# Performance work log

Measured on AMD Instinct MI355X. Metric: run time of the kernel, lower is better.

The kernel has to match this reference:

```python
import jax, jax.numpy as jnp
import numpy as np

B, C, H, W, HEADS = 8, 256, 64, 64, 4
EPS = 1e-5  # torch InstanceNorm2d default eps


def conv1x1(x, w):
    # w: [out_c, in_c]; x: [b, in_c, h, w]
    return jnp.einsum('oc,bchw->bohw', w, x)


def maxpool2(x):
    b, c, h, w = x.shape
    return x.reshape(b, c, h // 2, 2, w // 2, 2).max(axis=(3, 5))


def inorm_affine(x, g, b):
    # InstanceNorm2d(affine=True): normalize per (batch, channel) over H,W
    m = jnp.mean(x, axis=(2, 3), keepdims=True)
    v = jnp.mean((x - m) ** 2, axis=(2, 3), keepdims=True)
    return (x - m) * jax.lax.rsqrt(v + EPS) * g[None, :, None, None] + b[None, :, None, None]


def setup_inputs() -> dict:
    key = jax.random.key(0)
    ks = jax.random.split(key, 12)
    s = 1.0 / np.sqrt(C)  # fan-in style scaling for 1x1 conv weights
    return {
        'x': jax.random.normal(ks[0], (B, C, H, W), jnp.float32),
        'theta_w': jax.random.normal(ks[1], (C, C), jnp.float32) * s,
        'phi_w': jax.random.normal(ks[2], (C, C), jnp.float32) * s,
        'g_w': jax.random.normal(ks[3], (C // 2, C), jnp.float32) * s,
        'o_w': jax.random.normal(ks[4], (C, C // 2), jnp.float32) * np.sqrt(2.0 / C),
        'nt_w': 1.0 + 0.1 * jax.random.normal(ks[5], (C,), jnp.float32),
        'nt_b': 0.1 * jax.random.normal(ks[6], (C,), jnp.float32),
        'np_w': 1.0 + 0.1 * jax.random.normal(ks[7], (C,), jnp.float32),
        'np_b': 0.1 * jax.random.normal(ks[8], (C,), jnp.float32),
        'ng_w': 1.0 + 0.1 * jax.random.normal(ks[9], (C // 2,), jnp.float32),
        'ng_b': 0.1 * jax.random.normal(ks[10], (C // 2,), jnp.float32),
        'gamma': jnp.float32(0.5),
    }


def reference(x, theta_w, phi_w, g_w, o_w, nt_w, nt_b, np_w, np_b, ng_w, ng_b, gamma):
    b, c, h, w = x.shape
    n = h * w            # query length
    m = n // 4           # key/value length after 2x2 maxpool
    theta = inorm_affine(conv1x1(x, theta_w), nt_w, nt_b)
    phi = inorm_affine(maxpool2(conv1x1(x, phi_w)), np_w, np_b)
    g = inorm_affine(maxpool2(conv1x1(x, g_w)), ng_w, ng_b)
    # custom head layout: channel dim split as (C//heads, heads), head dim INNER
    theta_ = theta.reshape(b, c // HEADS, HEADS, n)
    phi_ = phi.reshape(b, c // HEADS, HEADS, m)
    g_ = g.reshape(b, (c // 2) // HEADS, HEADS, m)
    beta = jax.nn.softmax(jnp.einsum('bchi,bchj->bhij', theta_, phi_), axis=-1)
    o = jnp.einsum('bchj,bhij->bchi', g_, beta).reshape(b, c // 2, h, w)
    o = conv1x1(o, o_w)
    return gamma * o + x
```

## Files before the change

### kernel.cpp

```cpp
#include <hip/hip_runtime.h>
#include <hip/hip_bf16.h>
#include <math.h>

typedef float f32x4 __attribute__((ext_vector_type(4)));
typedef float f32x16 __attribute__((ext_vector_type(16)));
typedef __bf16 b16x8 __attribute__((ext_vector_type(8)));
typedef __bf16 b16x4 __attribute__((ext_vector_type(4)));
typedef unsigned int u32x2 __attribute__((ext_vector_type(2)));
typedef unsigned int u32x4 __attribute__((ext_vector_type(4)));

#define L2E 1.44269504088896340736f

__global__ void prep_weights(const float* tw, const float* pw, const float* gw,
                             const float* ow, __bf16* Wp, __bf16* OWp) {
    int idx = blockIdx.x * 256 + threadIdx.x;
    if (idx < 640 * 256) {
        int m = idx >> 8, k = idx & 255;
        float v;
        if (m < 256)      { int o = ((m & 63) << 2) + (m >> 6);            v = tw[o * 256 + k]; }
        else if (m < 512) { int mm = m - 256; int o = ((mm & 63) << 2) + (mm >> 6); v = pw[o * 256 + k]; }
        else              { int mm = m - 512; int o = ((mm & 31) << 2) + (mm >> 5); v = gw[o * 256 + k]; }
        Wp[idx] = (__bf16)v;
    } else {
        int j = idx - 640 * 256;
        if (j < 256 * 128) {
            int m = j >> 7, c = j & 127;
            int o = ((c & 31) << 2) + (c >> 5);
            OWp[j] = (__bf16)ow[m * 128 + o];
        }
    }
}

__global__ __launch_bounds__(256) void conv_gemm(const __bf16* __restrict__ Wp,
                                                 const float* __restrict__ x,
                                                 __bf16* theta_t, __bf16* phk, __bf16* gT,
                                                 float* tp1, float* tp2,
                                                 float* pp1, float* pp2,
                                                 float* gp1, float* gp2) {
    __shared__ __align__(16) char smem[38912];
    __bf16* Al = (__bf16*)smem;
    __bf16* Bl = (__bf16*)(smem + 10240);
    __bf16* Pl = (__bf16*)smem;
    float* S1w = (float*)(smem + 34816);
    float* S2w = (float*)(smem + 36864);
    int b = blockIdx.z, mt = blockIdx.y, nt = blockIdx.x;
    int tid = threadIdx.x, l = tid & 63, w = tid >> 6;
    int wm = w >> 1, wn = w & 1, lr = l & 15, lg = l >> 4;
    f32x4 acc[4][4];
#pragma unroll
    for (int i = 0; i < 4; i++)
#pragma unroll
        for (int j = 0; j < 4; j++)
#pragma unroll
            for (int r = 0; r < 4; r++) acc[i][j][r] = 0.f;
    const __bf16* Ag = Wp + (size_t)mt * 128 * 256;
    const float* Bx = x + (size_t)b * 1048576 + nt * 128;
    int srow = tid >> 2, scol = (tid & 3) * 8;
    int bn = tid & 127, bk0 = (tid >> 7) * 8;
    b16x8 aR[2];
    float xr[2][8];
#pragma unroll
    for (int hh = 0; hh < 2; hh++)
        aR[hh] = *(const b16x8*)&Ag[(size_t)(srow + hh * 64) * 256 + scol];
#pragma unroll
    for (int u = 0; u < 2; u++)
#pragma unroll
        for (int e = 0; e < 8; e++)
            xr[u][e] = Bx[(size_t)(bk0 + u * 16 + e) * 4096 + bn];
    for (int k0 = 0; k0 < 256; k0 += 32) {
        if (k0) __syncthreads();
#pragma unroll
        for (int hh = 0; hh < 2; hh++)
            *(b16x8*)&Al[(srow + hh * 64) * 40 + scol] = aR[hh];
#pragma unroll
        for (int u = 0; u < 2; u++) {
            b16x8 v;
#pragma unroll
            for (int e = 0; e < 8; e++) v[e] = (__bf16)xr[u][e];
            *(b16x8*)&Bl[bn * 40 + bk0 + u * 16] = v;
        }
        __syncthreads();
        if (k0 < 224) {
#pragma unroll
            for (int hh = 0; hh < 2; hh++)
                aR[hh] = *(const b16x8*)&Ag[(size_t)(srow + hh * 64) * 256 + k0 + 32 + scol];
#pragma unroll
            for (int u = 0; u < 2; u++)
#pragma unroll
                for (int e = 0; e < 8; e++)
                    xr[u][e] = Bx[(size_t)(k0 + 32 + bk0 + u * 16 + e) * 4096 + bn];
        }
        int ko = lg * 8;
        b16x8 af[4], bfr[4];
#pragma unroll
        for (int i = 0; i < 4; i++) af[i]  = *(b16x8*)&Al[(wm * 64 + i * 16 + lr) * 40 + ko];
#pragma unroll
        for (int i = 0; i < 4; i++) bfr[i] = *(b16x8*)&Bl[(wn * 64 + i * 16 + lr) * 40 + ko];
#pragma unroll
        for (int i = 0; i < 4; i++)
#pragma unroll
            for (int j = 0; j < 4; j++)
                acc[i][j] = __builtin_amdgcn_mfma_f32_16x16x32_bf16(af[i], bfr[j], acc[i][j], 0, 0, 0);
    }
    if (mt < 2) {
#pragma unroll
        for (int i = 0; i < 4; i++) {
            float s1v[4], s2v[4];
#pragma unroll
            for (int r = 0; r < 4; r++) {
                float a0 = acc[i][0][r], a1 = acc[i][1][r], a2 = acc[i][2][r], a3 = acc[i][3][r];
                s1v[r] = (a0 + a1) + (a2 + a3);
                s2v[r] = (a0 * a0 + a1 * a1) + (a2 * a2 + a3 * a3);
            }
#pragma unroll
            for (int msk = 1; msk < 16; msk <<= 1)
#pragma unroll
                for (int r = 0; r < 4; r++) {
                    s1v[r] += __shfl_xor(s1v[r], msk, 64);
                    s2v[r] += __shfl_xor(s2v[r], msk, 64);
                }
            if (lr == 0) {
                int row = (b * 32 + nt) * 2 + wn;
#pragma unroll
                for (int r = 0; r < 4; r++) {
                    int ch = mt * 128 + wm * 64 + i * 16 + lg * 4 + r;
                    tp1[row * 256 + ch] = s1v[r];
                    tp2[row * 256 + ch] = s2v[r];
                }
            }
        }
        int rbase = lg * 4;
#pragma unroll
        for (int i = 0; i < 4; i++) {
            int m = mt * 128 + wm * 64 + i * 16 + rbase;
#pragma unroll
            for (int j = 0; j < 4; j++) {
                int p = nt * 128 + wn * 64 + j * 16 + lr;
                b16x4 v;
#pragma unroll
                for (int r = 0; r < 4; r++) v[r] = (__bf16)acc[i][j][r];
                *(b16x4*)&theta_t[((size_t)b * 4096 + p) * 256 + m] = v;
            }
        }
    } else {
        __syncthreads();
        int rbase = lg * 4;
#pragma unroll
        for (int i = 0; i < 4; i++) {
            int ch = wm * 64 + i * 16 + rbase;
#pragma unroll
            for (int j = 0; j < 4; j++) {
                int p = wn * 64 + j * 16 + lr;
                b16x4 v;
#pragma unroll
                for (int r = 0; r < 4; r++) v[r] = (__bf16)acc[i][j][r];
                *(b16x4*)&Pl[p * 136 + ch] = v;
            }
        }
        __syncthreads();
        int o = tid & 15, tq = tid >> 4;
        float a1[8], a2[8];
#pragma unroll
        for (int e = 0; e < 8; e++) { a1[e] = 0.f; a2[e] = 0.f; }
        b16x8 pooled[2];
#pragma unroll
        for (int ss = 0; ss < 2; ss++) {
            int xq = tq * 2 + ss;
            b16x8 v0 = *(b16x8*)&Pl[(2 * xq) * 136 + o * 8];
            b16x8 v1 = *(b16x8*)&Pl[(2 * xq + 1) * 136 + o * 8];
            b16x8 v2 = *(b16x8*)&Pl[(64 + 2 * xq) * 136 + o * 8];
            b16x8 v3 = *(b16x8*)&Pl[(65 + 2 * xq) * 136 + o * 8];
            b16x8 mv;
#pragma unroll
            for (int e = 0; e < 8; e++) {
                float m = fmaxf(fmaxf((float)v0[e], (float)v1[e]), fmaxf((float)v2[e], (float)v3[e]));
                mv[e] = (__bf16)m; a1[e] += m; a2[e] += m * m;
            }
            pooled[ss] = mv;
        }
#pragma unroll
        for (int e = 0; e < 8; e++) {
            a1[e] += __shfl_xor(a1[e], 16, 64); a1[e] += __shfl_xor(a1[e], 32, 64);
            a2[e] += __shfl_xor(a2[e], 16, 64); a2[e] += __shfl_xor(a2[e], 32, 64);
        }
        if ((tid & 63) < 16) {
#pragma unroll
            for (int e = 0; e < 8; e++) {
                S1w[w * 128 + o * 8 + e] = a1[e];
                S2w[w * 128 + o * 8 + e] = a2[e];
            }
        }
        __syncthreads();
        int cc = nt >> 1;
        if (mt < 4) {
            if (tid < 128) {
                float s1 = S1w[tid] + S1w[128 + tid] + S1w[256 + tid] + S1w[384 + tid];
                float s2 = S2w[tid] + S2w[128 + tid] + S2w[256 + tid] + S2w[384 + tid];
                pp1[(size_t)(b * 32 + nt) * 256 + (mt - 2) * 128 + tid] = s1;
                pp2[(size_t)(b * 32 + nt) * 256 + (mt - 2) * 128 + tid] = s2;
            }
            int hh = (mt - 2) * 2 + (o >> 3), slot = o & 7, bh = b * 4 + hh;
#pragma unroll
            for (int ss = 0; ss < 2; ss++) {
                int key = (nt & 1) * 32 + tq * 2 + ss;
                *(b16x8*)&phk[((((size_t)bh * 16 + cc) * 8 + slot) * 64 + key) * 8] = pooled[ss];
            }
        } else {
            if (tid < 128) {
                float s1 = S1w[tid] + S1w[128 + tid] + S1w[256 + tid] + S1w[384 + tid];
                float s2 = S2w[tid] + S2w[128 + tid] + S2w[256 + tid] + S2w[384 + tid];
                gp1[(size_t)(b * 32 + nt) * 128 + tid] = s1;
                gp2[(size_t)(b * 32 + nt) * 128 + tid] = s2;
            }
            __bf16* Pg = Pl;
#pragma unroll
            for (int ss = 0; ss < 2; ss++)
                *(b16x8*)&Pg[(tq * 2 + ss) * 136 + o * 8] = pooled[ss];
            __syncthreads();
            int ch = tid & 127, kg = tid >> 7;
            int hh = ch >> 5, c32 = ch & 31, bh = b * 4 + hh;
#pragma unroll
            for (int gi = 0; gi < 2; gi++) {
                int g2 = kg * 2 + gi;
                b16x8 v;
#pragma unroll
                for (int e = 0; e < 8; e++) v[e] = Pg[(g2 * 8 + e) * 136 + ch];
                int seg = (nt & 1) * 4 + g2;
                *(b16x8*)&gT[((((size_t)bh * 16 + cc) * 8 + seg) * 32 + c32) * 8] = v;
            }
        }
    }
}

__global__ void finalize_stats(const float* tp1, const float* tp2, const float* pp1,
                               const float* pp2, const float* gp1, const float* gp2,
                               const float* ntw, const float* ntb, const float* npw,
                               const float* npb, const float* ngw, const float* ngb,
                               float* sct, float* bit, float* scp, float* bip,
                               float* scg, float* big) {
    int idx = blockIdx.x * 256 + threadIdx.x;
    if (idx >= 8 * 640) return;
    int b = idx / 640, c = idx % 640;
    if (c < 256) {
        float s1 = 0.f, s2 = 0.f;
        for (int i = 0; i < 64; i++) { s1 += tp1[(b * 64 + i) * 256 + c]; s2 += tp2[(b * 64 + i) * 256 + c]; }
        float n = 4096.f;
        float m = s1 / n, v = s2 / n - m * m;
        float r = rsqrtf(v + 1e-5f);
        int o = ((c & 63) << 2) + (c >> 6);
        float wv = ntw[o], bv = ntb[o];
        sct[b * 256 + c] = r * wv * L2E;
        bit[b * 256 + c] = (bv - m * r * wv) * L2E;
    } else if (c < 512) {
        int cc = c - 256;
        float s1 = 0.f, s2 = 0.f;
        for (int i = 0; i < 32; i++) { s1 += pp1[(b * 32 + i) * 256 + cc]; s2 += pp2[(b * 32 + i) * 256 + cc]; }
        float n = 1024.f;
        float m = s1 / n, v = s2 / n - m * m;
        float r = rsqrtf(v + 1e-5f);
        int o = ((cc & 63) << 2) + (cc >> 6);
        float wv = npw[o], bv = npb[o];
        scp[b * 256 + cc] = r * wv; bip[b * 256 + cc] = bv - m * r * wv;
    } else {
        int cc = c - 512;
        float s1 = 0.f, s2 = 0.f;
        for (int i = 0; i < 32; i++) { s1 += gp1[(b * 32 + i) * 128 + cc]; s2 += gp2[(b * 32 + i) * 128 + cc]; }
        float n = 1024.f;
        float m = s1 / n, v = s2 / n - m * m;
        float r = rsqrtf(v + 1e-5f);
        int o = ((cc & 31) << 2) + (cc >> 5);
        float wv = ngw[o], bv = ngb[o];
        scg[b * 128 + cc] = r * wv; big[b * 128 + cc] = bv - m * r * wv;
    }
}

__global__ void normalize_phk(__bf16* __restrict__ phk,
                              const float* __restrict__ scp,
                              const float* __restrict__ bip) {
    int u = blockIdx.x * 256 + threadIdx.x;
    int bh = u >> 13, slot = (u >> 6) & 7;
    int b = bh >> 2, h = bh & 3;
    int cf = b * 256 + h * 64 + (slot >> 1) * 16 + (slot & 1) * 8;
    size_t off = (size_t)u * 8;
    b16x8 v = *(b16x8*)&phk[off];
    b16x8 nv;
#pragma unroll
    for (int e = 0; e < 8; e++)
        nv[e] = (__bf16)((float)v[e] * scp[cf + e] + bip[cf + e]);
    *(b16x8*)&phk[off] = nv;
}

__global__ __launch_bounds__(256, 2) void attn(const __bf16* __restrict__ theta_t,
                                               const __bf16* __restrict__ phk,
                                               const __bf16* __restrict__ gTz,
                                               const float* __restrict__ sct,
                                               const float* __restrict__ bit,
                                               const float* __restrict__ scg,
                                               const float* __restrict__ big,
                                               __bf16* __restrict__ o_mid) {
    int bid = blockIdx.x;
    int idx = bid >> 3;
    int bh = (bid & 7) * 4 + (idx >> 4), qt = idx & 15;
    int b = bh >> 2, h = bh & 3;
    int tid = threadIdx.x, w = tid >> 6, lane = tid & 63;
    int l31 = lane & 31, hi = lane >> 5;
    int qb = qt * 256 + w * 64;

    b16x8 qf[2][4];
#pragma unroll
    for (int m = 0; m < 2; m++) {
        int q = qb + m * 32 + l31;
        const __bf16* qp = theta_t + ((size_t)b * 4096 + q) * 256 + h * 64;
#pragma unroll
        for (int st = 0; st < 4; st++) {
            int cb = st * 16 + hi * 8;
            b16x8 raw = *(const b16x8*)&qp[cb];
            b16x8 nv;
#pragma unroll
            for (int e = 0; e < 8; e++) {
                int cix = b * 256 + h * 64 + cb + e;
                nv[e] = (__bf16)((float)raw[e] * sct[cix] + bit[cix]);
            }
            qf[m][st] = nv;
        }
    }

    const __bf16* Kg = phk + (size_t)bh * 65536 + (size_t)hi * 512 + (size_t)l31 * 8;
    const __bf16* Vg = gTz + (size_t)bh * 32768 + (size_t)hi * 256 + (size_t)l31 * 8;

    f32x16 oacc[2];
    float l_run[2] = {0.f, 0.f};
#pragma unroll
    for (int m = 0; m < 2; m++)
#pragma unroll
        for (int r = 0; r < 16; r++) oacc[m][r] = 0.f;
    f32x16 zc;
#pragma unroll
    for (int r = 0; r < 16; r++) zc[r] = 0.f;

    b16x8 akA[2][4], avA[4], akB[2][4], avB[4];

#define LOADK(dst, c) { _Pragma("unroll") for (int kf = 0; kf < 2; kf++) \
    _Pragma("unroll") for (int st = 0; st < 4; st++) \
        dst[kf][st] = *(const b16x8*)&Kg[(size_t)(c) * 4096 + st * 1024 + kf * 256]; }
#define LOADV(dst, c) { _Pragma("unroll") for (int js = 0; js < 4; js++) \
    dst[js] = *(const b16x8*)&Vg[(size_t)(c) * 2048 + js * 512]; }
#define COMPUTE(ak, av) { \
    _Pragma("unroll") for (int m = 0; m < 2; m++) { \
        _Pragma("unroll") for (int kf = 0; kf < 2; kf++) { \
            f32x16 s = __builtin_amdgcn_mfma_f32_32x32x16_bf16(ak[kf][0], qf[m][0], zc, 0, 0, 0); \
            _Pragma("unroll") for (int st = 1; st < 4; st++) \
                s = __builtin_amdgcn_mfma_f32_32x32x16_bf16(ak[kf][st], qf[m][st], s, 0, 0, 0); \
            float sum = 0.f; \
            _Pragma("unroll") for (int r = 0; r < 16; r++) { \
                float p = __builtin_amdgcn_exp2f(s[r]); s[r] = p; sum += p; } \
            l_run[m] += sum; \
            _Pragma("unroll") for (int hh2 = 0; hh2 < 2; hh2++) { \
                b16x4 A4, B4; \
                _Pragma("unroll") for (int e = 0; e < 4; e++) { \
                    A4[e] = (__bf16)s[hh2 * 8 + e]; B4[e] = (__bf16)s[hh2 * 8 + 4 + e]; } \
                u32x2 a2 = __builtin_bit_cast(u32x2, A4); \
                u32x2 b2 = __builtin_bit_cast(u32x2, B4); \
                u32x2 q0 = __builtin_amdgcn_permlane32_swap(a2[0], b2[0], false, false); \
                u32x2 q1 = __builtin_amdgcn_permlane32_swap(a2[1], b2[1], false, false); \
                u32x4 pd = {q0[0], q1[0], q0[1], q1[1]}; \
                b16x8 pf = __builtin_bit_cast(b16x8, pd); \
                oacc[m] = __builtin_amdgcn_mfma_f32_32x32x16_bf16(av[kf * 2 + hh2], pf, oacc[m], 0, 0, 0); \
            } \
        } \
    } }

    LOADK(akA, 0) LOADV(avA, 0)
#pragma unroll 1
    for (int c = 0; c < 16; c += 2) {
        LOADK(akB, c + 1) LOADV(avB, c + 1)
        COMPUTE(akA, avA)
        if (c + 2 < 16) { LOADK(akA, c + 2) LOADV(avA, c + 2) }
        COMPUTE(akB, avB)
    }
#undef LOADK
#undef LOADV
#undef COMPUTE

#pragma unroll
    for (int m = 0; m < 2; m++) {
        float lr = l_run[m] + __shfl_xor(l_run[m], 32, 64);
        float rl = 1.0f / lr;
        int q = qb + m * 32 + l31;
#pragma unroll
        for (int rr = 0; rr < 4; rr++) {
            b16x4 v;
#pragma unroll
            for (int e = 0; e < 4; e++) {
                int ci = b * 128 + h * 32 + rr * 8 + hi * 4 + e;
                v[e] = (__bf16)(oacc[m][rr * 4 + e] * rl * scg[ci] + big[ci]);
            }
            *(b16x4*)&o_mid[((size_t)b * 4096 + q) * 128 + h * 32 + rr * 8 + hi * 4] = v;
        }
    }
}

__global__ __launch_bounds__(256) void out_gemm(const __bf16* __restrict__ OWp,
                                                const __bf16* __restrict__ o_mid,
                                                const float* __restrict__ x,
                                                const float* gamma, float* out) {
    int b = blockIdx.z, mt = blockIdx.y, nt = blockIdx.x;
    __shared__ __bf16 Al[128 * 40];
    __shared__ __bf16 Bl[128 * 40];
    int tid = threadIdx.x, l = tid & 63, w = tid >> 6;
    int wm = w >> 1, wn = w & 1, lr = l & 15, lg = l >> 4;
    f32x4 acc[4][4];
#pragma unroll
    for (int i = 0; i < 4; i++)
#pragma unroll
        for (int j = 0; j < 4; j++)
#pragma unroll
            for (int r = 0; r < 4; r++) acc[i][j][r] = 0.f;
    const __bf16* Ag = OWp + (size_t)mt * 128 * 128;
    const __bf16* Bg = o_mid + ((size_t)b * 4096 + nt * 128) * 128;
    int srow = tid >> 2, scol = (tid & 3) * 8;
    b16x8 aR[2], bR[2];
#pragma unroll
    for (int hh = 0; hh < 2; hh++) {
        int r = srow + hh * 64;
        aR[hh] = *(const b16x8*)&Ag[(size_t)r * 128 + scol];
        bR[hh] = *(const b16x8*)&Bg[(size_t)r * 128 + scol];
    }
    for (int k0 = 0; k0 < 128; k0 += 32) {
        if (k0) __syncthreads();
#pragma unroll
        for (int hh = 0; hh < 2; hh++) {
            int r = srow + hh * 64;
            *(b16x8*)&Al[r * 40 + scol] = aR[hh];
            *(b16x8*)&Bl[r * 40 + scol] = bR[hh];
        }
        __syncthreads();
        if (k0 < 96) {
#pragma unroll
            for (int hh = 0; hh < 2; hh++) {
                int r = srow + hh * 64;
                aR[hh] = *(const b16x8*)&Ag[(size_t)r * 128 + k0 + 32 + scol];
                bR[hh] = *(const b16x8*)&Bg[(size_t)r * 128 + k0 + 32 + scol];
            }
        }
        int ko = lg * 8;
        b16x8 af[4], bfr[4];
#pragma unroll
        for (int i = 0; i < 4; i++) af[i]  = *(b16x8*)&Al[(wm * 64 + i * 16 + lr) * 40 + ko];
#pragma unroll
        for (int i = 0; i < 4; i++) bfr[i] = *(b16x8*)&Bl[(wn * 64 + i * 16 + lr) * 40 + ko];
#pragma unroll
        for (int i = 0; i < 4; i++)
#pragma unroll
            for (int j = 0; j < 4; j++)
                acc[i][j] = __builtin_amdgcn_mfma_f32_16x16x32_bf16(af[i], bfr[j], acc[i][j], 0, 0, 0);
    }
    float gm = gamma[0];
    int rbase = lg * 4;
#pragma unroll
    for (int i = 0; i < 4; i++) {
        int m = mt * 128 + wm * 64 + i * 16 + rbase;
#pragma unroll
        for (int j = 0; j < 4; j++) {
            int p = nt * 128 + wn * 64 + j * 16 + lr;
#pragma unroll
            for (int r = 0; r < 4; r++) {
                size_t o = ((size_t)b * 256 + m + r) * 4096 + p;
                __builtin_nontemporal_store(gm * acc[i][j][r] + x[o], &out[o]);
            }
        }
    }
}

extern "C" void kernel_launch(void* const* d_in, const int* in_sizes, int n_in,
                              void* d_out, int out_size, void* d_ws, size_t ws_size,
                              hipStream_t stream) {
    const float* x   = (const float*)d_in[0];
    const float* tw  = (const float*)d_in[1];
    const float* pw  = (const float*)d_in[2];
    const float* gw  = (const float*)d_in[3];
    const float* ow  = (const float*)d_in[4];
    const float* ntw = (const float*)d_in[5];
    const float* ntb = (const float*)d_in[6];
    const float* npw = (const float*)d_in[7];
    const float* npb = (const float*)d_in[8];
    const float* ngw = (const float*)d_in[9];
    const float* ngb = (const float*)d_in[10];
    const float* gamma = (const float*)d_in[11];
    float* out = (float*)d_out;
    char* ws = (char*)d_ws;

    __bf16* Wp  = (__bf16*)(ws + 0);
    __bf16* OWp = (__bf16*)(ws + 327680);
    float* tp1  = (float*)(ws + 393216);
    float* tp2  = (float*)(ws + 917504);
    float* pp1  = (float*)(ws + 1441792);
    float* pp2  = (float*)(ws + 1703936);
    float* gp1  = (float*)(ws + 1966080);
    float* gp2  = (float*)(ws + 2097152);
    float* sb   = (float*)(ws + 2228224);
    __bf16* th  = (__bf16*)(ws + 2269184);
    __bf16* phk = (__bf16*)(ws + 19046400);
    __bf16* gT  = (__bf16*)(ws + 23240704);
    __bf16* om  = (__bf16*)(ws + 25337856);

    float *sct = sb, *bit = sb + 2048, *scp = sb + 4096, *bip = sb + 6144,
          *scg = sb + 8192, *big = sb + 9216;

    prep_weights<<<768, 256, 0, stream>>>(tw, pw, gw, ow, Wp, OWp);
    conv_gemm<<<dim3(32, 5, 8), 256, 0, stream>>>(Wp, x, th, phk, gT,
                                                  tp1, tp2, pp1, pp2, gp1, gp2);
    finalize_stats<<<20, 256, 0, stream>>>(tp1, tp2, pp1, pp2, gp1, gp2,
                                           ntw, ntb, npw, npb, ngw, ngb,
                                           sct, bit, scp, bip, scg, big);
    normalize_phk<<<1024, 256, 0, stream>>>(phk, scp, bip);
    attn<<<512, 256, 0, stream>>>(th, phk, gT, sct, bit, scg, big, om);
    out_gemm<<<dim3(32, 2, 8), 256, 0, stream>>>(OWp, om, x, gamma, out);
}
```

Measured before the change: 105.2 us.

## Swizzle GEMM LDS tiles and split pooling epilogue into two rounds

Replaces the padded stride-40 LDS layout in conv_gemm and out_gemm with an unpadded stride-32 layout that XOR-swizzles 16-byte chunks by row, aiming to keep bank conflicts low while using less shared memory. The pooling epilogue for phi/g now stages half of the accumulator tile per round in a smaller buffer, writing pooled keys and transposed g directly each round. This shrinks conv_gemm LDS from about 38KB to 25KB, which may allow more resident blocks, at the cost of extra barriers. Key ordering in the phi/g outputs changes, and the normalization kernel's channel mapping is adjusted to match.

```diff
diff --git a/kernel.cpp b/kernel.cpp
--- a/kernel.cpp
+++ b/kernel.cpp
@@ -10,6 +10,7 @@
 typedef unsigned int u32x4 __attribute__((ext_vector_type(4)));
 
 #define L2E 1.44269504088896340736f
+#define BADDR(row, oct) (((row) << 5) + ((((oct) ^ ((row) & 3))) << 3))
 
 __global__ void prep_weights(const float* tw, const float* pw, const float* gw,
                              const float* ow, __bf16* Wp, __bf16* OWp) {
@@ -37,12 +38,13 @@
                                                  float* tp1, float* tp2,
                                                  float* pp1, float* pp2,
                                                  float* gp1, float* gp2) {
-    __shared__ __align__(16) char smem[38912];
-    __bf16* Al = (__bf16*)smem;
-    __bf16* Bl = (__bf16*)(smem + 10240);
-    __bf16* Pl = (__bf16*)smem;
-    float* S1w = (float*)(smem + 34816);
-    float* S2w = (float*)(smem + 36864);
+    __shared__ __align__(16) char smem[25856];
+    __bf16* Al  = (__bf16*)smem;
+    __bf16* Bl  = (__bf16*)(smem + 8192);
+    __bf16* Pl  = (__bf16*)smem;
+    float*  S1w = (float*)(smem + 17408);
+    float*  S2w = (float*)(smem + 19456);
+    __bf16* Pg  = (__bf16*)(smem + 21504);
     int b = blockIdx.z, mt = blockIdx.y, nt = blockIdx.x;
     int tid = threadIdx.x, l = tid & 63, w = tid >> 6;
     int wm = w >> 1, wn = w & 1, lr = l & 15, lg = l >> 4;
@@ -55,47 +57,46 @@
             for (int r = 0; r < 4; r++) acc[i][j][r] = 0.f;
     const __bf16* Ag = Wp + (size_t)mt * 128 * 256;
     const float* Bx = x + (size_t)b * 1048576 + nt * 128;
-    int srow = tid >> 2, scol = (tid & 3) * 8;
-    int bn = tid & 127, bk0 = (tid >> 7) * 8;
+    int srow = tid >> 2, so = tid & 3;
+    int bn = tid & 127, bo = tid >> 7;
     b16x8 aR[2];
     float xr[2][8];
 #pragma unroll
     for (int hh = 0; hh < 2; hh++)
-        aR[hh] = *(const b16x8*)&Ag[(size_t)(srow + hh * 64) * 256 + scol];
+        aR[hh] = *(const b16x8*)&Ag[(size_t)(srow + hh * 64) * 256 + so * 8];
 #pragma unroll
     for (int u = 0; u < 2; u++)
 #pragma unroll
         for (int e = 0; e < 8; e++)
-            xr[u][e] = Bx[(size_t)(bk0 + u * 16 + e) * 4096 + bn];
+            xr[u][e] = Bx[(size_t)((bo + u * 2) * 8 + e) * 4096 + bn];
     for (int k0 = 0; k0 < 256; k0 += 32) {
         if (k0) __syncthreads();
 #pragma unroll
         for (int hh = 0; hh < 2; hh++)
-            *(b16x8*)&Al[(srow + hh * 64) * 40 + scol] = aR[hh];
+            *(b16x8*)&Al[BADDR(srow + hh * 64, so)] = aR[hh];
 #pragma unroll
         for (int u = 0; u < 2; u++) {
             b16x8 v;
 #pragma unroll
             for (int e = 0; e < 8; e++) v[e] = (__bf16)xr[u][e];
-            *(b16x8*)&Bl[bn * 40 + bk0 + u * 16] = v;
+            *(b16x8*)&Bl[BADDR(bn, bo + u * 2)] = v;
         }
         __syncthreads();
         if (k0 < 224) {
 #pragma unroll
             for (int hh = 0; hh < 2; hh++)
-                aR[hh] = *(const b16x8*)&Ag[(size_t)(srow + hh * 64) * 256 + k0 + 32 + scol];
+                aR[hh] = *(const b16x8*)&Ag[(size_t)(srow + hh * 64) * 256 + k0 + 32 + so * 8];
 #pragma unroll
             for (int u = 0; u < 2; u++)
 #pragma unroll
                 for (int e = 0; e < 8; e++)
-                    xr[u][e] = Bx[(size_t)(k0 + 32 + bk0 + u * 16 + e) * 4096 + bn];
-        }
-        int ko = lg * 8;
+                    xr[u][e] = Bx[(size_t)(k0 + 32 + (bo + u * 2) * 8 + e) * 4096 + bn];
+        }
         b16x8 af[4], bfr[4];
 #pragma unroll
-        for (int i = 0; i < 4; i++) af[i]  = *(b16x8*)&Al[(wm * 64 + i * 16 + lr) * 40 + ko];
-#pragma unroll
-        for (int i = 0; i < 4; i++) bfr[i] = *(b16x8*)&Bl[(wn * 64 + i * 16 + lr) * 40 + ko];
+        for (int i = 0; i < 4; i++) af[i]  = *(b16x8*)&Al[BADDR(wm * 64 + i * 16 + lr, lg)];
+#pragma unroll
+        for (int i = 0; i < 4; i++) bfr[i] = *(b16x8*)&Bl[BADDR(wn * 64 + i * 16 + lr, lg)];
 #pragma unroll
         for (int i = 0; i < 4; i++)
 #pragma unroll
@@ -143,40 +144,53 @@
             }
         }
     } else {
-        __syncthreads();
-        int rbase = lg * 4;
-#pragma unroll
-        for (int i = 0; i < 4; i++) {
-            int ch = wm * 64 + i * 16 + rbase;
-#pragma unroll
-            for (int j = 0; j < 4; j++) {
-                int p = wn * 64 + j * 16 + lr;
-                b16x4 v;
-#pragma unroll
-                for (int r = 0; r < 4; r++) v[r] = (__bf16)acc[i][j][r];
-                *(b16x4*)&Pl[p * 136 + ch] = v;
-            }
-        }
-        __syncthreads();
+        int cc = nt >> 1;
         int o = tid & 15, tq = tid >> 4;
         float a1[8], a2[8];
 #pragma unroll
         for (int e = 0; e < 8; e++) { a1[e] = 0.f; a2[e] = 0.f; }
-        b16x8 pooled[2];
-#pragma unroll
-        for (int ss = 0; ss < 2; ss++) {
-            int xq = tq * 2 + ss;
-            b16x8 v0 = *(b16x8*)&Pl[(2 * xq) * 136 + o * 8];
-            b16x8 v1 = *(b16x8*)&Pl[(2 * xq + 1) * 136 + o * 8];
-            b16x8 v2 = *(b16x8*)&Pl[(64 + 2 * xq) * 136 + o * 8];
-            b16x8 v3 = *(b16x8*)&Pl[(65 + 2 * xq) * 136 + o * 8];
-            b16x8 mv;
+#pragma unroll 1
+        for (int rnd = 0; rnd < 2; rnd++) {
+            __syncthreads();
+#pragma unroll
+            for (int i = 0; i < 4; i++) {
+                int ch = wm * 64 + i * 16 + lg * 4;
+#pragma unroll
+                for (int jj = 0; jj < 2; jj++) {
+                    int j = rnd * 2 + jj;
+                    int lrow = jj * 16 + lr + wn * 32;
+                    b16x4 v;
+#pragma unroll
+                    for (int r = 0; r < 4; r++) v[r] = (__bf16)acc[i][j][r];
+                    *(b16x4*)&Pl[lrow * 136 + ch] = v;
+                }
+            }
+            __syncthreads();
+            b16x8 v0 = *(b16x8*)&Pl[(2 * tq) * 136 + o * 8];
+            b16x8 v1 = *(b16x8*)&Pl[(2 * tq + 1) * 136 + o * 8];
+            b16x8 v2 = *(b16x8*)&Pl[(32 + 2 * tq) * 136 + o * 8];
+            b16x8 v3 = *(b16x8*)&Pl[(33 + 2 * tq) * 136 + o * 8];
+            b16x8 pooled;
 #pragma unroll
             for (int e = 0; e < 8; e++) {
                 float m = fmaxf(fmaxf((float)v0[e], (float)v1[e]), fmaxf((float)v2[e], (float)v3[e]));
-                mv[e] = (__bf16)m; a1[e] += m; a2[e] += m * m;
-            }
-            pooled[ss] = mv;
+                pooled[e] = (__bf16)m; a1[e] += m; a2[e] += m * m;
+            }
+            if (mt < 4) {
+                int key = (nt & 1) * 32 + rnd * 16 + tq;
+                int hh = (mt - 2) * 2 + (o >> 3), slot = o & 7, bh = b * 4 + hh;
+                *(b16x8*)&phk[((((size_t)bh * 16 + cc) * 8 + slot) * 64 + key) * 8] = pooled;
+            } else {
+                *(b16x8*)&Pg[tq * 136 + o * 8] = pooled;
+                __syncthreads();
+                int ch = tid & 127, kg = tid >> 7;
+                int hh = ch >> 5, c32 = ch & 31, bh = b * 4 + hh;
+                b16x8 v;
+#pragma unroll
+                for (int e = 0; e < 8; e++) v[e] = Pg[(kg * 8 + e) * 136 + ch];
+                int seg = (nt & 1) * 4 + rnd * 2 + kg;
+                *(b16x8*)&gT[((((size_t)bh * 16 + cc) * 8 + seg) * 32 + c32) * 8] = v;
+            }
         }
 #pragma unroll
         for (int e = 0; e < 8; e++) {
@@ -191,42 +205,15 @@
             }
         }
         __syncthreads();
-        int cc = nt >> 1;
-        if (mt < 4) {
-            if (tid < 128) {
-                float s1 = S1w[tid] + S1w[128 + tid] + S1w[256 + tid] + S1w[384 + tid];
-                float s2 = S2w[tid] + S2w[128 + tid] + S2w[256 + tid] + S2w[384 + tid];
+        if (tid < 128) {
+            float s1 = S1w[tid] + S1w[128 + tid] + S1w[256 + tid] + S1w[384 + tid];
+            float s2 = S2w[tid] + S2w[128 + tid] + S2w[256 + tid] + S2w[384 + tid];
+            if (mt < 4) {
                 pp1[(size_t)(b * 32 + nt) * 256 + (mt - 2) * 128 + tid] = s1;
                 pp2[(size_t)(b * 32 + nt) * 256 + (mt - 2) * 128 + tid] = s2;
-            }
-            int hh = (mt - 2) * 2 + (o >> 3), slot = o & 7, bh = b * 4 + hh;
-#pragma unroll
-            for (int ss = 0; ss < 2; ss++) {
-                int key = (nt & 1) * 32 + tq * 2 + ss;
-                *(b16x8*)&phk[((((size_t)bh * 16 + cc) * 8 + slot) * 64 + key) * 8] = pooled[ss];
-            }
-        } else {
-            if (tid < 128) {
-                float s1 = S1w[tid] + S1w[128 + tid] + S1w[256 + tid] + S1w[384 + tid];
-                float s2 = S2w[tid] + S2w[128 + tid] + S2w[256 + tid] + S2w[384 + tid];
+            } else {
                 gp1[(size_t)(b * 32 + nt) * 128 + tid] = s1;
                 gp2[(size_t)(b * 32 + nt) * 128 + tid] = s2;
-            }
-            __bf16* Pg = Pl;
-#pragma unroll
-            for (int ss = 0; ss < 2; ss++)
-                *(b16x8*)&Pg[(tq * 2 + ss) * 136 + o * 8] = pooled[ss];
-            __syncthreads();
-            int ch = tid & 127, kg = tid >> 7;
-            int hh = ch >> 5, c32 = ch & 31, bh = b * 4 + hh;
-#pragma unroll
-            for (int gi = 0; gi < 2; gi++) {
-                int g2 = kg * 2 + gi;
-                b16x8 v;
-#pragma unroll
-                for (int e = 0; e < 8; e++) v[e] = Pg[(g2 * 8 + e) * 136 + ch];
-                int seg = (nt & 1) * 4 + g2;
-                *(b16x8*)&gT[((((size_t)bh * 16 + cc) * 8 + seg) * 32 + c32) * 8] = v;
             }
         }
     }
@@ -280,7 +267,7 @@
     int u = blockIdx.x * 256 + threadIdx.x;
     int bh = u >> 13, slot = (u >> 6) & 7;
     int b = bh >> 2, h = bh & 3;
-    int cf = b * 256 + h * 64 + (slot >> 1) * 16 + (slot & 1) * 8;
+    int cf = b * 256 + h * 64 + slot * 8;
     size_t off = (size_t)u * 8;
     b16x8 v = *(b16x8*)&phk[off];
     b16x8 nv;
@@ -405,8 +392,8 @@
                                                 const float* __restrict__ x,
                                                 const float* gamma, float* out) {
     int b = blockIdx.z, mt = blockIdx.y, nt = blockIdx.x;
-    __shared__ __bf16 Al[128 * 40];
-    __shared__ __bf16 Bl[128 * 40];
+    __shared__ __bf16 Al[128 * 32];
+    __shared__ __bf16 Bl[128 * 32];
     int tid = threadIdx.x, l = tid & 63, w = tid >> 6;
     int wm = w >> 1, wn = w & 1, lr = l & 15, lg = l >> 4;
     f32x4 acc[4][4];
@@ -418,37 +405,36 @@
             for (int r = 0; r < 4; r++) acc[i][j][r] = 0.f;
     const __bf16* Ag = OWp + (size_t)mt * 128 * 128;
     const __bf16* Bg = o_mid + ((size_t)b * 4096 + nt * 128) * 128;
-    int srow = tid >> 2, scol = (tid & 3) * 8;
+    int srow = tid >> 2, so = tid & 3;
     b16x8 aR[2], bR[2];
 #pragma unroll
     for (int hh = 0; hh < 2; hh++) {
         int r = srow + hh * 64;
-        aR[hh] = *(const b16x8*)&Ag[(size_t)r * 128 + scol];
-        bR[hh] = *(const b16x8*)&Bg[(size_t)r * 128 + scol];
+        aR[hh] = *(const b16x8*)&Ag[(size_t)r * 128 + so * 8];
+        bR[hh] = *(const b16x8*)&Bg[(size_t)r * 128 + so * 8];
     }
     for (int k0 = 0; k0 < 128; k0 += 32) {
         if (k0) __syncthreads();
 #pragma unroll
         for (int hh = 0; hh < 2; hh++) {
             int r = srow + hh * 64;
-            *(b16x8*)&Al[r * 40 + scol] = aR[hh];
-            *(b16x8*)&Bl[r * 40 + scol] = bR[hh];
+            *(b16x8*)&Al[BADDR(r, so)] = aR[hh];
+            *(b16x8*)&Bl[BADDR(r, so)] = bR[hh];
         }
         __syncthreads();
         if (k0 < 96) {
 #pragma unroll
             for (int hh = 0; hh < 2; hh++) {
                 int r = srow + hh * 64;
-                aR[hh] = *(const b16x8*)&Ag[(size_t)r * 128 + k0 + 32 + scol];
-                bR[hh] = *(const b16x8*)&Bg[(size_t)r * 128 + k0 + 32 + scol];
-            }
-        }
-        int ko = lg * 8;
+                aR[hh] = *(const b16x8*)&Ag[(size_t)r * 128 + k0 + 32 + so * 8];
+                bR[hh] = *(const b16x8*)&Bg[(size_t)r * 128 + k0 + 32 + so * 8];
+            }
+        }
         b16x8 af[4], bfr[4];
 #pragma unroll
-        for (int i = 0; i < 4; i++) af[i]  = *(b16x8*)&Al[(wm * 64 + i * 16 + lr) * 40 + ko];
-#pragma unroll
-        for (int i = 0; i < 4; i++) bfr[i] = *(b16x8*)&Bl[(wn * 64 + i * 16 + lr) * 40 + ko];
+        for (int i = 0; i < 4; i++) af[i]  = *(b16x8*)&Al[BADDR(wm * 64 + i * 16 + lr, lg)];
+#pragma unroll
+        for (int i = 0; i < 4; i++) bfr[i] = *(b16x8*)&Bl[BADDR(wn * 64 + i * 16 + lr, lg)];
 #pragma unroll
         for (int i = 0; i < 4; i++)
 #pragma unroll
```

Result: slower. 183.4 us (+74.4%).
